# Kernel optimization log

Measured on AMD Instinct MI355X. Metric: run time of the kernel, lower is better.

Reference implementation:

```python
import jax, jax.numpy as jnp
import numpy as np

F8_MAX = 448.0  # float8_e4m3fn max
F4_MAX = 6.0    # fp4 e2m1 max
BLOCK = 16      # NVFP4 scaling block size along K

# representable |values| of fp4 e2m1 and midpoints for nearest rounding
_LEVELS = jnp.array([0.0, 0.5, 1.0, 1.5, 2.0, 3.0, 4.0, 6.0], dtype=jnp.float32)
_MIDS = (_LEVELS[:-1] + _LEVELS[1:]) * 0.5


def _e2m1_round(a):
    # round-to-nearest fp4 e2m1 value, sign-magnitude
    s = jnp.sign(a)
    m = jnp.clip(jnp.abs(a), 0.0, F4_MAX)
    idx = jnp.searchsorted(_MIDS, m, side='left')
    return s * jnp.take(_LEVELS, idx)


def _e4m3(x):
    # quantize to float8 e4m3 and dequantize back to fp32
    return jnp.clip(x, -F8_MAX, F8_MAX).astype(jnp.float8_e4m3fn).astype(jnp.float32)


def nvfp4_fake_quant(x, s2):
    # x: [..., K]; s2: scalar global scale = 448*6/global_amax
    shp = x.shape
    K = shp[-1]
    xb = x.reshape(shp[:-1] + (K // BLOCK, BLOCK))  # [..., K/16, 16]
    amax = jnp.max(jnp.abs(xb), axis=-1, keepdims=True)
    sf = _e4m3(amax * s2 / F4_MAX)          # stored per-block fp8 scale (cutlass_vec)
    scale = sf / s2                          # per-block dequant scale in real units
    safe = jnp.where(scale > 0.0, scale, 1.0)
    q = _e2m1_round(xb / safe)               # fp4 codes (as values)
    deq = jnp.where(scale > 0.0, q * scale, 0.0)
    return deq.reshape(shp)


def setup_inputs() -> dict:
    key = jax.random.key(0)
    kx, kw, kb, ks = jax.random.split(key, 4)
    K, N = 4096, 4096
    x = jax.random.normal(kx, (4, 2048, K), dtype=jnp.float32)
    weight = jax.random.uniform(kw, (N, K), dtype=jnp.float32)
    bias = jax.random.uniform(kb, (N,), dtype=jnp.float32)
    # fp4_global_scale of a rand(1, K) tensor, as done in the module __init__
    dummy = jax.random.uniform(ks, (1, K), dtype=jnp.float32)
    s_in2 = ((F8_MAX * F4_MAX) / jnp.max(jnp.abs(dummy))).reshape(1)
    return {'x': x, 'weight': weight, 'bias': bias, 's_in2': s_in2}


def reference(x, weight, bias, s_in2):
    s2_in = s_in2.reshape(())
    s2_w = (F8_MAX * F4_MAX) / jnp.max(jnp.abs(weight))  # fp4_global_scale(weight)
    x_dq = nvfp4_fake_quant(x, s2_in)        # fake-quant activations
    w_dq = nvfp4_fake_quant(weight, s2_w)    # dequantized fp4 weight (stored at init)
    # F.linear: [b,s,k] @ [n,k]^T + bias
    return jnp.einsum('bsk,nk->bsn', x_dq, w_dq) + bias
```

## Files before the change

kernel.cpp:

```cpp
#include <hip/hip_runtime.h>
#include <hip/hip_bf16.h>

typedef __attribute__((ext_vector_type(8))) short short8;
typedef __attribute__((ext_vector_type(8))) unsigned short ushort8;
typedef __attribute__((ext_vector_type(4))) float f32x4;
typedef unsigned short ushort;

#define K_DIM 4096
#define N_DIM 4096
#define BK 32
#define NT_TILES (K_DIM / BK)


__device__ __forceinline__ float e4m3_rne(float v) {
    if (v >= 0.015625f) {
        unsigned u = __float_as_uint(v);
        unsigned lsb = (u >> 20) & 1u;
        u = (u + 0x7FFFFu + lsb) & 0xFFF00000u;
        return __uint_as_float(u);
    }
    return rintf(v * 512.0f) * 0.001953125f;
}

__device__ __forceinline__ float e2m1_level(float m) {
    float lv = 0.0f;
    lv = (m > 0.25f) ? 0.5f : lv;
    lv = (m > 0.75f) ? 1.0f : lv;
    lv = (m > 1.25f) ? 1.5f : lv;
    lv = (m > 1.75f) ? 2.0f : lv;
    lv = (m > 2.5f)  ? 3.0f : lv;
    lv = (m > 3.5f)  ? 4.0f : lv;
    lv = (m > 5.0f)  ? 6.0f : lv;
    return lv;
}

__device__ __forceinline__ ushort f32_to_bf16_bits(float f) {
    unsigned u = __float_as_uint(f);
    return (ushort)((u + 0x7FFFu + ((u >> 16) & 1u)) >> 16);
}


__global__ void wamax_kernel(const float* __restrict__ w, unsigned* amax_bits, int n4) {
    float m = 0.f;
    const f32x4* w4 = (const f32x4*)w;
    for (int i = blockIdx.x * blockDim.x + threadIdx.x; i < n4; i += gridDim.x * blockDim.x) {
        f32x4 v = w4[i];
        m = fmaxf(m, fmaxf(fmaxf(fabsf(v.x), fabsf(v.y)), fmaxf(fabsf(v.z), fabsf(v.w))));
    }
#pragma unroll
    for (int off = 32; off >= 1; off >>= 1)
        m = fmaxf(m, __shfl_down(m, off));
    __shared__ float red[4];
    const int lane = threadIdx.x & 63, wv = threadIdx.x >> 6;
    if (lane == 0) red[wv] = m;
    __syncthreads();
    if (threadIdx.x == 0) {
        m = fmaxf(fmaxf(red[0], red[1]), fmaxf(red[2], red[3]));
        atomicMax(amax_bits, __float_as_uint(m));
    }
}

__global__ void quant16_kernel(const float* __restrict__ src,
                               const float* __restrict__ s2_ptr,
                               const unsigned* __restrict__ amax_bits,
                               ushort* __restrict__ dst, int nblk) {
    int t = blockIdx.x * blockDim.x + threadIdx.x;
    if (t >= nblk) return;
    float s2;
    if (s2_ptr) s2 = *s2_ptr;
    else        s2 = 2688.0f / __uint_as_float(*amax_bits);

    const f32x4* s = (const f32x4*)src + (size_t)t * 4;
    float vals[16];
    f32x4 v0 = s[0], v1 = s[1], v2 = s[2], v3 = s[3];
#pragma unroll
    for (int i = 0; i < 4; ++i) {
        vals[i] = v0[i]; vals[4 + i] = v1[i]; vals[8 + i] = v2[i]; vals[12 + i] = v3[i];
    }
    float amax = 0.f;
#pragma unroll
    for (int i = 0; i < 16; ++i) amax = fmaxf(amax, fabsf(vals[i]));

    float sf = e4m3_rne(fminf(amax * s2 / 6.0f, 448.0f));
    float scale = sf / s2;

    ushort8 o0, o1;
    if (scale > 0.f) {
#pragma unroll
        for (int i = 0; i < 16; ++i) {
            float r = vals[i] / scale;
            float m = fminf(fabsf(r), 6.0f);
            float q = copysignf(e2m1_level(m), r);
            ushort b = f32_to_bf16_bits(q * scale);
            if (i < 8) o0[i] = b; else o1[i - 8] = b;
        }
    } else {
#pragma unroll
        for (int i = 0; i < 8; ++i) { o0[i] = 0; o1[i] = 0; }
    }
    ushort8* d8 = (ushort8*)(dst + (size_t)t * 16);
    d8[0] = o0;
    d8[1] = o1;
}


__device__ __forceinline__ void gload16(const ushort* g, ushort* l) {
    __builtin_amdgcn_global_load_lds(
        (const __attribute__((address_space(1))) void*)g,
        (__attribute__((address_space(3))) void*)l, 16, 0, 0);
}

#define SYNC(N)                                              \
    asm volatile("s_waitcnt vmcnt(" #N ")" ::: "memory");    \
    __builtin_amdgcn_sched_barrier(0);                       \
    __builtin_amdgcn_s_barrier();                            \
    __builtin_amdgcn_sched_barrier(0)

__global__ __launch_bounds__(512, 2) void gemm8(
    const ushort* __restrict__ Aq, const ushort* __restrict__ Bq,
    const float* __restrict__ bias, float* __restrict__ C) {
    __shared__ ushort lds[4 * 16384];

    const int tid  = threadIdx.x;
    const int lane = tid & 63;
    const int wave = tid >> 6;
    const int wr = wave >> 2;
    const int wc = wave & 3;

    const int swz = blockIdx.x;
    const int g = swz >> 8, l = swz & 255;
    const int by = g * 16 + (l & 15);
    const int bx = l >> 4;
    const int bm = by * 256, bn = bx * 256;

    const int r0  = tid >> 2;
    const int cg0 = ((tid & 3) - ((r0 >> 1) & 3)) & 3;
    const ushort* sA0 = Aq + (size_t)(bm + r0) * K_DIM + cg0 * 8;
    const ushort* sB0 = Bq + (size_t)(bn + r0) * K_DIM + cg0 * 8;
    ushort* dA0 = &lds[wave * 512];
    ushort* dB0 = &lds[8192 + wave * 512];

    const int pr   = ((lane >> 4) + ((lane & 15) >> 1)) & 3;
    const int idxA = (wr * 128 + (lane & 15)) * 32 + pr * 8;
    const int idxB = 8192 + (wc * 64 + (lane & 15)) * 32 + pr * 8;

    f32x4 acc[8][4];
#pragma unroll
    for (int m = 0; m < 8; ++m)
#pragma unroll
        for (int n = 0; n < 4; ++n) acc[m][n] = (f32x4)(0.f);

#define STAGE(t) {                                                         \
        const size_t ko = (size_t)(t) * BK;                                \
        const int bb = ((t) & 3) * 16384;                                  \
        gload16(sA0 + ko,                          dA0 + bb);              \
        gload16(sA0 + (size_t)128 * K_DIM + ko,    dA0 + bb + 4096);       \
        gload16(sB0 + ko,                          dB0 + bb);              \
        gload16(sB0 + (size_t)128 * K_DIM + ko,    dB0 + bb + 4096); }

    auto compute = [&](int bufo) {
        const ushort* Lb = &lds[bufo];
        short8 af[8], bfr[4];
#pragma unroll
        for (int m = 0; m < 8; ++m) af[m]  = *(const short8*)(Lb + idxA + m * 512);
#pragma unroll
        for (int n = 0; n < 4; ++n) bfr[n] = *(const short8*)(Lb + idxB + n * 512);
#pragma unroll
        for (int m = 0; m < 8; ++m)
#pragma unroll
            for (int n = 0; n < 4; ++n)
                acc[m][n] = __builtin_amdgcn_mfma_f32_16x16x32_bf16(af[m], bfr[n], acc[m][n], 0, 0, 0);
    };

    STAGE(0); STAGE(1); STAGE(2);
    SYNC(8);

    for (int t = 0; t < NT_TILES - 3; ++t) {
        STAGE(t + 3);
        compute((t & 3) * 16384);
        SYNC(8);
    }
    compute(((NT_TILES - 3) & 3) * 16384);
    SYNC(4);
    compute(((NT_TILES - 2) & 3) * 16384);
    SYNC(0);
    compute(((NT_TILES - 1) & 3) * 16384);

    const int fq = lane >> 4, fr = lane & 15;
    float bv[4];
#pragma unroll
    for (int n = 0; n < 4; ++n) bv[n] = bias[bn + wc * 64 + n * 16 + fr];
#pragma unroll
    for (int m = 0; m < 8; ++m)
#pragma unroll
        for (int r = 0; r < 4; ++r) {
            const int row = bm + wr * 128 + m * 16 + fq * 4 + r;
            float* Cr = C + (size_t)row * N_DIM + bn + wc * 64 + fr;
#pragma unroll
            for (int n = 0; n < 4; ++n) Cr[n * 16] = acc[m][n][r] + bv[n];
        }
#undef STAGE
}


extern "C" void kernel_launch(void* const* d_in, const int* in_sizes, int n_in,
                              void* d_out, int out_size, void* d_ws, size_t ws_size,
                              hipStream_t stream) {
    const float* x     = (const float*)d_in[0];
    const float* w     = (const float*)d_in[1];
    const float* bias  = (const float*)d_in[2];
    const float* s_in2 = (const float*)d_in[3];
    float* out = (float*)d_out;

    const int M = in_sizes[0] / K_DIM;

    unsigned* amax_bits = (unsigned*)d_ws;
    ushort* xq = (ushort*)((char*)d_ws + 256);
    ushort* wq = (ushort*)((char*)d_ws + 256 + (size_t)M * K_DIM * 2);

    hipMemsetAsync(amax_bits, 0, 4, stream);
    wamax_kernel<<<1024, 256, 0, stream>>>(w, amax_bits, (N_DIM * K_DIM) / 4);

    const int nblk_x = (M * K_DIM) / 16;
    quant16_kernel<<<nblk_x / 256, 256, 0, stream>>>(x, s_in2, nullptr, xq, nblk_x);
    const int nblk_w = (N_DIM * K_DIM) / 16;
    quant16_kernel<<<nblk_w / 256, 256, 0, stream>>>(w, nullptr, amax_bits, wq, nblk_w);

    const int nwg = (M / 256) * (N_DIM / 256);
    gemm8<<<nwg, 512, 0, stream>>>(xq, wq, bias, out);
}
```

Measured before the change: 310.1 us.

## Restructure bf16 GEMM into double-buffered BK=64 pipeline with interleaved quarter-tile loads

The GEMM main loop moves from a 4-stage BK=32 ring buffer to a 2-stage BK=64 double buffer. Each K-tile's compute is split into four quadrant MFMA groups, and each group is interleaved with a quarter of the next tile's global-to-LDS loads plus fine-grained waitcnt and barriers. MFMA sections are raised in priority with s_setprio. The wave-to-output mapping changes to split 64-row by 32-col quadrants, with an 8-way XOR-like LDS swizzle for the wider tile. The aim is better overlap of memory and MFMA work and fewer barriers per unit of K, at the cost of more barriers per tile and less prefetch depth.

```diff
diff --git a/kernel.cpp b/kernel.cpp
--- a/kernel.cpp
+++ b/kernel.cpp
@@ -8,8 +8,8 @@
 
 #define K_DIM 4096
 #define N_DIM 4096
-#define BK 32
-#define NT_TILES (K_DIM / BK)
+#define BK 64
+#define NT (K_DIM / BK)
 
 
 __device__ __forceinline__ float e4m3_rne(float v) {
@@ -110,16 +110,15 @@
         (__attribute__((address_space(3))) void*)l, 16, 0, 0);
 }
 
-#define SYNC(N)                                              \
-    asm volatile("s_waitcnt vmcnt(" #N ")" ::: "memory");    \
-    __builtin_amdgcn_sched_barrier(0);                       \
-    __builtin_amdgcn_s_barrier();                            \
-    __builtin_amdgcn_sched_barrier(0)
+#define VM4 asm volatile("s_waitcnt vmcnt(4)" ::: "memory")
+#define VM2 asm volatile("s_waitcnt vmcnt(2)" ::: "memory")
+#define VM0 asm volatile("s_waitcnt vmcnt(0)" ::: "memory")
+#define BAR asm volatile("s_barrier" ::: "memory")
 
 __global__ __launch_bounds__(512, 2) void gemm8(
     const ushort* __restrict__ Aq, const ushort* __restrict__ Bq,
     const float* __restrict__ bias, float* __restrict__ C) {
-    __shared__ ushort lds[4 * 16384];
+    __shared__ ushort lds[2 * 32768];
 
     const int tid  = threadIdx.x;
     const int lane = tid & 63;
@@ -128,21 +127,24 @@
     const int wc = wave & 3;
 
     const int swz = blockIdx.x;
-    const int g = swz >> 8, l = swz & 255;
-    const int by = g * 16 + (l & 15);
-    const int bx = l >> 4;
+    const int grp = swz >> 8, lcl = swz & 255;
+    const int by = grp * 16 + (lcl & 15);
+    const int bx = lcl >> 4;
     const int bm = by * 256, bn = bx * 256;
 
-    const int r0  = tid >> 2;
-    const int cg0 = ((tid & 3) - ((r0 >> 1) & 3)) & 3;
-    const ushort* sA0 = Aq + (size_t)(bm + r0) * K_DIM + cg0 * 8;
-    const ushort* sB0 = Bq + (size_t)(bn + r0) * K_DIM + cg0 * 8;
-    ushort* dA0 = &lds[wave * 512];
-    ushort* dB0 = &lds[8192 + wave * 512];
-
-    const int pr   = ((lane >> 4) + ((lane & 15) >> 1)) & 3;
-    const int idxA = (wr * 128 + (lane & 15)) * 32 + pr * 8;
-    const int idxB = 8192 + (wc * 64 + (lane & 15)) * 32 + pr * 8;
+    const int r0  = tid >> 3;
+    const int cg0 = ((tid & 7) - ((r0 >> 1) & 7)) & 7;
+    const ushort* sA = Aq + (size_t)(bm + r0) * K_DIM + cg0 * 8;
+    const ushort* sB = Bq + (size_t)(bn + r0) * K_DIM + cg0 * 8;
+    ushort* dst0 = &lds[tid * 8];
+
+    const int rowA = wr * 64 + (lane & 15);
+    const int rowB = wc * 32 + (lane & 15);
+    const int ksl  = lane >> 4;
+    const int baseA[2] = { rowA * 64 + ((((ksl) + (rowA >> 1)) & 7) << 3),
+                           rowA * 64 + (((4 + ksl + (rowA >> 1)) & 7) << 3) };
+    const int baseB[2] = { 16384 + rowB * 64 + ((((ksl) + (rowB >> 1)) & 7) << 3),
+                           16384 + rowB * 64 + (((4 + ksl + (rowB >> 1)) & 7) << 3) };
 
     f32x4 acc[8][4];
 #pragma unroll
@@ -150,56 +152,102 @@
 #pragma unroll
         for (int n = 0; n < 4; ++n) acc[m][n] = (f32x4)(0.f);
 
-#define STAGE(t) {                                                         \
-        const size_t ko = (size_t)(t) * BK;                                \
-        const int bb = ((t) & 3) * 16384;                                  \
-        gload16(sA0 + ko,                          dA0 + bb);              \
-        gload16(sA0 + (size_t)128 * K_DIM + ko,    dA0 + bb + 4096);       \
-        gload16(sB0 + ko,                          dB0 + bb);              \
-        gload16(sB0 + (size_t)128 * K_DIM + ko,    dB0 + bb + 4096); }
-
-    auto compute = [&](int bufo) {
-        const ushort* Lb = &lds[bufo];
-        short8 af[8], bfr[4];
-#pragma unroll
-        for (int m = 0; m < 8; ++m) af[m]  = *(const short8*)(Lb + idxA + m * 512);
-#pragma unroll
-        for (int n = 0; n < 4; ++n) bfr[n] = *(const short8*)(Lb + idxB + n * 512);
-#pragma unroll
-        for (int m = 0; m < 8; ++m)
+    short8 af[4][2], bfr[4][2];
+
+#define SA0(t) { const size_t ko = (size_t)(t) * BK; ushort* d = dst0 + ((t) & 1) * 32768;         \
+    gload16(sA + ko, d); gload16(sA + (size_t)64 * K_DIM + ko, d + 4096); }
+#define SA1(t) { const size_t ko = (size_t)(t) * BK; ushort* d = dst0 + ((t) & 1) * 32768 + 8192;  \
+    gload16(sA + (size_t)128 * K_DIM + ko, d); gload16(sA + (size_t)192 * K_DIM + ko, d + 4096); }
+#define SB0(t) { const size_t ko = (size_t)(t) * BK; ushort* d = dst0 + ((t) & 1) * 32768 + 16384; \
+    gload16(sB + ko, d); gload16(sB + (size_t)64 * K_DIM + ko, d + 4096); }
+#define SB1(t) { const size_t ko = (size_t)(t) * BK; ushort* d = dst0 + ((t) & 1) * 32768 + 24576; \
+    gload16(sB + (size_t)128 * K_DIM + ko, d); gload16(sB + (size_t)192 * K_DIM + ko, d + 4096); }
+
+#define READ_A(mh, Lb)                                                        \
+    _Pragma("unroll") for (int m = 0; m < 4; ++m) {                           \
+        af[m][0] = *(const short8*)((Lb) + (mh) * 8192 + m * 1024 + baseA[0]); \
+        af[m][1] = *(const short8*)((Lb) + (mh) * 8192 + m * 1024 + baseA[1]); }
+#define READ_B(nh, Lb)                                                        \
+    _Pragma("unroll") for (int n = 0; n < 2; ++n) {                           \
+        bfr[(nh)*2 + n][0] = *(const short8*)((Lb) + (nh) * 8192 + n * 1024 + baseB[0]); \
+        bfr[(nh)*2 + n][1] = *(const short8*)((Lb) + (nh) * 8192 + n * 1024 + baseB[1]); }
+
+#define MM(m0, n0)                                                            \
+    __builtin_amdgcn_s_setprio(1);                                            \
+    _Pragma("unroll") for (int m = 0; m < 4; ++m)                             \
+    _Pragma("unroll") for (int n = 0; n < 2; ++n)                             \
+    _Pragma("unroll") for (int ks = 0; ks < 2; ++ks)                          \
+        acc[(m0) + m][(n0) + n] = __builtin_amdgcn_mfma_f32_16x16x32_bf16(    \
+            af[m][ks], bfr[(n0) + n][ks], acc[(m0) + m][(n0) + n], 0, 0, 0);  \
+    __builtin_amdgcn_s_setprio(0);
+
+    SA0(0); SB0(0); SB1(0); SA1(0);
+    VM4; BAR;
+
+#pragma unroll 1
+    for (int t = 0; t < NT - 1; ++t) {
+        const ushort* Lb = &lds[(t & 1) * 32768];
+        READ_A(0, Lb); READ_B(0, Lb);
+        SA0(t + 1);
+        VM4; BAR;
+        MM(0, 0);
+        BAR;
+        READ_B(1, Lb);
+        SB0(t + 1);
+        VM4; BAR;
+        MM(0, 2);
+        BAR;
+        READ_A(1, Lb);
+        SB1(t + 1);
+        BAR;
+        MM(4, 0);
+        BAR;
+        SA1(t + 1);
+        VM4; BAR;
+        MM(4, 2);
+        BAR;
+    }
+    {
+        const ushort* Lb = &lds[((NT - 1) & 1) * 32768];
+        READ_A(0, Lb); READ_B(0, Lb);
+        VM2; BAR;
+        MM(0, 0);
+        BAR;
+        READ_B(1, Lb);
+        VM0; BAR;
+        MM(0, 2);
+        BAR;
+        READ_A(1, Lb);
+        BAR;
+        MM(4, 0);
+        BAR;
+        BAR;
+        MM(4, 2);
+        BAR;
+    }
+
+    const int fq = lane >> 4, fr = lane & 15;
+    const int colb = bn + wc * 32 + fr;
+    float bv[4];
+#pragma unroll
+    for (int n = 0; n < 4; ++n) bv[n] = bias[colb + (n >> 1) * 128 + (n & 1) * 16];
+#pragma unroll
+    for (int m = 0; m < 8; ++m)
+#pragma unroll
+        for (int r = 0; r < 4; ++r) {
+            const int row = bm + (m >> 2) * 128 + wr * 64 + (m & 3) * 16 + fq * 4 + r;
+            float* Cr = C + (size_t)row * N_DIM + colb;
 #pragma unroll
             for (int n = 0; n < 4; ++n)
-                acc[m][n] = __builtin_amdgcn_mfma_f32_16x16x32_bf16(af[m], bfr[n], acc[m][n], 0, 0, 0);
-    };
-
-    STAGE(0); STAGE(1); STAGE(2);
-    SYNC(8);
-
-    for (int t = 0; t < NT_TILES - 3; ++t) {
-        STAGE(t + 3);
-        compute((t & 3) * 16384);
-        SYNC(8);
-    }
-    compute(((NT_TILES - 3) & 3) * 16384);
-    SYNC(4);
-    compute(((NT_TILES - 2) & 3) * 16384);
-    SYNC(0);
-    compute(((NT_TILES - 1) & 3) * 16384);
-
-    const int fq = lane >> 4, fr = lane & 15;
-    float bv[4];
-#pragma unroll
-    for (int n = 0; n < 4; ++n) bv[n] = bias[bn + wc * 64 + n * 16 + fr];
-#pragma unroll
-    for (int m = 0; m < 8; ++m)
-#pragma unroll
-        for (int r = 0; r < 4; ++r) {
-            const int row = bm + wr * 128 + m * 16 + fq * 4 + r;
-            float* Cr = C + (size_t)row * N_DIM + bn + wc * 64 + fr;
-#pragma unroll
-            for (int n = 0; n < 4; ++n) Cr[n * 16] = acc[m][n][r] + bv[n];
+                Cr[(n >> 1) * 128 + (n & 1) * 16] = acc[m][n][r] + bv[n];
         }
-#undef STAGE
+#undef SA0
+#undef SA1
+#undef SB0
+#undef SB1
+#undef READ_A
+#undef READ_B
+#undef MM
 }
 
 
```

New measurement: 322.3 us. 4.0% more time.

## Software-pipeline LDS fragment reads with MFMA halves and split global loads

Applied to the files above, without the earlier changes.

Restructures the GEMM main loop so the LDS fragment reads for the next half-tile and tile are issued while the current MFMA half runs. The code uses finer lgkmcnt and vmcnt waits, a single barrier per tile, and interleaves the A and B global-to-LDS loads between the two MFMA halves. It also raises wave priority around the MFMA blocks with s_setprio. The intent is to hide LDS read latency and reduce barrier stalls. The cost is more fragile wait-count reasoning and a possible race on buffer reuse.

```diff
diff --git a/kernel.cpp b/kernel.cpp
--- a/kernel.cpp
+++ b/kernel.cpp
@@ -9,7 +9,7 @@
 #define K_DIM 4096
 #define N_DIM 4096
 #define BK 32
-#define NT_TILES (K_DIM / BK)
+#define NT (K_DIM / BK)
 
 
 __device__ __forceinline__ float e4m3_rne(float v) {
@@ -110,11 +110,13 @@
         (__attribute__((address_space(3))) void*)l, 16, 0, 0);
 }
 
-#define SYNC(N)                                              \
-    asm volatile("s_waitcnt vmcnt(" #N ")" ::: "memory");    \
-    __builtin_amdgcn_sched_barrier(0);                       \
-    __builtin_amdgcn_s_barrier();                            \
-    __builtin_amdgcn_sched_barrier(0)
+#define VM4 asm volatile("s_waitcnt vmcnt(4)" ::: "memory")
+#define VM0 asm volatile("s_waitcnt vmcnt(0)" ::: "memory")
+#define LG4 do { asm volatile("s_waitcnt lgkmcnt(4)" ::: "memory"); \
+                 __builtin_amdgcn_sched_barrier(0); } while (0)
+#define LG0 do { asm volatile("s_waitcnt lgkmcnt(0)" ::: "memory"); \
+                 __builtin_amdgcn_sched_barrier(0); } while (0)
+#define BAR asm volatile("s_barrier" ::: "memory")
 
 __global__ __launch_bounds__(512, 2) void gemm8(
     const ushort* __restrict__ Aq, const ushort* __restrict__ Bq,
@@ -128,9 +130,9 @@
     const int wc = wave & 3;
 
     const int swz = blockIdx.x;
-    const int g = swz >> 8, l = swz & 255;
-    const int by = g * 16 + (l & 15);
-    const int bx = l >> 4;
+    const int grp = swz >> 8, lcl = swz & 255;
+    const int by = grp * 16 + (lcl & 15);
+    const int bx = lcl >> 4;
     const int bm = by * 256, bn = bx * 256;
 
     const int r0  = tid >> 2;
@@ -150,41 +152,78 @@
 #pragma unroll
         for (int n = 0; n < 4; ++n) acc[m][n] = (f32x4)(0.f);
 
-#define STAGE(t) {                                                         \
-        const size_t ko = (size_t)(t) * BK;                                \
-        const int bb = ((t) & 3) * 16384;                                  \
-        gload16(sA0 + ko,                          dA0 + bb);              \
-        gload16(sA0 + (size_t)128 * K_DIM + ko,    dA0 + bb + 4096);       \
-        gload16(sB0 + ko,                          dB0 + bb);              \
-        gload16(sB0 + (size_t)128 * K_DIM + ko,    dB0 + bb + 4096); }
-
-    auto compute = [&](int bufo) {
-        const ushort* Lb = &lds[bufo];
-        short8 af[8], bfr[4];
-#pragma unroll
-        for (int m = 0; m < 8; ++m) af[m]  = *(const short8*)(Lb + idxA + m * 512);
-#pragma unroll
-        for (int n = 0; n < 4; ++n) bfr[n] = *(const short8*)(Lb + idxB + n * 512);
-#pragma unroll
-        for (int m = 0; m < 8; ++m)
-#pragma unroll
-            for (int n = 0; n < 4; ++n)
-                acc[m][n] = __builtin_amdgcn_mfma_f32_16x16x32_bf16(af[m], bfr[n], acc[m][n], 0, 0, 0);
-    };
-
-    STAGE(0); STAGE(1); STAGE(2);
-    SYNC(8);
-
-    for (int t = 0; t < NT_TILES - 3; ++t) {
-        STAGE(t + 3);
-        compute((t & 3) * 16384);
-        SYNC(8);
-    }
-    compute(((NT_TILES - 3) & 3) * 16384);
-    SYNC(4);
-    compute(((NT_TILES - 2) & 3) * 16384);
-    SYNC(0);
-    compute(((NT_TILES - 1) & 3) * 16384);
+    short8 af[8], bfr[4];
+
+#define SA(t) { const size_t ko = (size_t)(t) * BK; const int bb = ((t) & 3) * 16384; \
+    gload16(sA0 + ko, dA0 + bb); gload16(sA0 + (size_t)128 * K_DIM + ko, dA0 + bb + 4096); }
+#define SB(t) { const size_t ko = (size_t)(t) * BK; const int bb = ((t) & 3) * 16384; \
+    gload16(sB0 + ko, dB0 + bb); gload16(sB0 + (size_t)128 * K_DIM + ko, dB0 + bb + 4096); }
+
+#define READ_ALO(bb) _Pragma("unroll") for (int m = 0; m < 4; ++m) \
+        af[m] = *(const short8*)&lds[(bb) + idxA + m * 512];
+#define READ_AHI(bb) _Pragma("unroll") for (int m = 0; m < 4; ++m) \
+        af[4 + m] = *(const short8*)&lds[(bb) + idxA + (4 + m) * 512];
+#define READ_B(bb)   _Pragma("unroll") for (int n = 0; n < 4; ++n) \
+        bfr[n] = *(const short8*)&lds[(bb) + idxB + n * 512];
+
+#define MML                                                                   \
+    __builtin_amdgcn_s_setprio(1);                                            \
+    _Pragma("unroll") for (int m = 0; m < 4; ++m)                             \
+    _Pragma("unroll") for (int n = 0; n < 4; ++n)                             \
+        acc[m][n] = __builtin_amdgcn_mfma_f32_16x16x32_bf16(af[m], bfr[n], acc[m][n], 0, 0, 0); \
+    __builtin_amdgcn_s_setprio(0);
+#define MMH                                                                   \
+    __builtin_amdgcn_s_setprio(1);                                            \
+    _Pragma("unroll") for (int m = 4; m < 8; ++m)                             \
+    _Pragma("unroll") for (int n = 0; n < 4; ++n)                             \
+        acc[m][n] = __builtin_amdgcn_mfma_f32_16x16x32_bf16(af[m], bfr[n], acc[m][n], 0, 0, 0); \
+    __builtin_amdgcn_s_setprio(0);
+
+    SA(0); SB(0); SA(1); SB(1); SA(2); SB(2);
+    VM4; BAR;
+    READ_ALO(0); READ_B(0);
+
+#pragma unroll 1
+    for (int t = 0; t <= NT - 4; ++t) {
+        const int bb  = (t & 3) * 16384;
+        const int bb1 = ((t + 1) & 3) * 16384;
+        VM4; BAR;
+        READ_AHI(bb);
+        SA(t + 3);
+        LG4;
+        MML;
+        READ_ALO(bb1);
+        SB(t + 3);
+        LG4;
+        MMH;
+        READ_B(bb1);
+    }
+    {
+        const int bb  = ((NT - 3) & 3) * 16384;
+        const int bb1 = ((NT - 2) & 3) * 16384;
+        VM4; BAR;
+        READ_AHI(bb);
+        LG4; MML;
+        READ_ALO(bb1);
+        LG4; MMH;
+        READ_B(bb1);
+    }
+    {
+        const int bb  = ((NT - 2) & 3) * 16384;
+        const int bb1 = ((NT - 1) & 3) * 16384;
+        VM0; BAR;
+        READ_AHI(bb);
+        LG4; MML;
+        READ_ALO(bb1);
+        LG4; MMH;
+        READ_B(bb1);
+    }
+    {
+        const int bb = ((NT - 1) & 3) * 16384;
+        READ_AHI(bb);
+        LG4; MML;
+        LG0; MMH;
+    }
 
     const int fq = lane >> 4, fr = lane & 15;
     float bv[4];
@@ -199,7 +238,13 @@
 #pragma unroll
             for (int n = 0; n < 4; ++n) Cr[n * 16] = acc[m][n][r] + bv[n];
         }
-#undef STAGE
+#undef SA
+#undef SB
+#undef READ_ALO
+#undef READ_AHI
+#undef READ_B
+#undef MML
+#undef MMH
 }
 
 
```

Result: faster. 297.7 us (-4.0%).

## Shrink GEMM tile to 128x256 with 3-stage LDS pipeline and interleaved MFMA waits

Applied to the files above, without the earlier changes.

Halves the M tile to 128 rows, giving each wave a 4x4 MFMA accumulator, and drops from a 4-buffer to a 3-buffer LDS ring so occupancy can rise to 4 workgroups per CU. The main loop is restructured so LDS fragment reads are issued before the next global-to-LDS stage, and MFMAs are split into groups gated by lgkmcnt waits with setprio raised around them. This targets better latency hiding and occupancy, at the cost of lower arithmetic intensity per tile, since B tiles are reloaded twice as often.

```diff
diff --git a/kernel.cpp b/kernel.cpp
--- a/kernel.cpp
+++ b/kernel.cpp
@@ -9,7 +9,7 @@
 #define K_DIM 4096
 #define N_DIM 4096
 #define BK 32
-#define NT_TILES (K_DIM / BK)
+#define NT (K_DIM / BK)
 
 
 __device__ __forceinline__ float e4m3_rne(float v) {
@@ -110,16 +110,19 @@
         (__attribute__((address_space(3))) void*)l, 16, 0, 0);
 }
 
-#define SYNC(N)                                              \
-    asm volatile("s_waitcnt vmcnt(" #N ")" ::: "memory");    \
-    __builtin_amdgcn_sched_barrier(0);                       \
-    __builtin_amdgcn_s_barrier();                            \
-    __builtin_amdgcn_sched_barrier(0)
-
-__global__ __launch_bounds__(512, 2) void gemm8(
+#define VM3 asm volatile("s_waitcnt vmcnt(3)" ::: "memory")
+#define VM0 asm volatile("s_waitcnt vmcnt(0)" ::: "memory")
+#define LGW(N) do { asm volatile("s_waitcnt lgkmcnt(" #N ")" ::: "memory"); \
+                    __builtin_amdgcn_sched_barrier(0); } while (0)
+#define BAR asm volatile("s_barrier" ::: "memory")
+
+#define BUFSZ 12288
+#define BOFF_B 4096
+
+__global__ __launch_bounds__(512, 4) void gemm8(
     const ushort* __restrict__ Aq, const ushort* __restrict__ Bq,
     const float* __restrict__ bias, float* __restrict__ C) {
-    __shared__ ushort lds[4 * 16384];
+    __shared__ ushort lds[3 * BUFSZ];
 
     const int tid  = threadIdx.x;
     const int lane = tid & 63;
@@ -128,78 +131,97 @@
     const int wc = wave & 3;
 
     const int swz = blockIdx.x;
-    const int g = swz >> 8, l = swz & 255;
-    const int by = g * 16 + (l & 15);
-    const int bx = l >> 4;
-    const int bm = by * 256, bn = bx * 256;
+    const int grp = swz >> 8, lcl = swz & 255;
+    const int by = grp * 16 + (lcl & 15);
+    const int bx = lcl >> 4;
+    const int bm = by * 128, bn = bx * 256;
 
     const int r0  = tid >> 2;
     const int cg0 = ((tid & 3) - ((r0 >> 1) & 3)) & 3;
     const ushort* sA0 = Aq + (size_t)(bm + r0) * K_DIM + cg0 * 8;
     const ushort* sB0 = Bq + (size_t)(bn + r0) * K_DIM + cg0 * 8;
-    ushort* dA0 = &lds[wave * 512];
-    ushort* dB0 = &lds[8192 + wave * 512];
+    ushort* dA0 = &lds[tid * 8];
+    ushort* dB0 = &lds[BOFF_B + tid * 8];
 
     const int pr   = ((lane >> 4) + ((lane & 15) >> 1)) & 3;
-    const int idxA = (wr * 128 + (lane & 15)) * 32 + pr * 8;
-    const int idxB = 8192 + (wc * 64 + (lane & 15)) * 32 + pr * 8;
-
-    f32x4 acc[8][4];
-#pragma unroll
-    for (int m = 0; m < 8; ++m)
+    const int idxA = (wr * 64 + (lane & 15)) * 32 + pr * 8;
+    const int idxB = BOFF_B + (wc * 64 + (lane & 15)) * 32 + pr * 8;
+
+    f32x4 acc[4][4];
+#pragma unroll
+    for (int m = 0; m < 4; ++m)
 #pragma unroll
         for (int n = 0; n < 4; ++n) acc[m][n] = (f32x4)(0.f);
 
-#define STAGE(t) {                                                         \
-        const size_t ko = (size_t)(t) * BK;                                \
-        const int bb = ((t) & 3) * 16384;                                  \
-        gload16(sA0 + ko,                          dA0 + bb);              \
-        gload16(sA0 + (size_t)128 * K_DIM + ko,    dA0 + bb + 4096);       \
-        gload16(sB0 + ko,                          dB0 + bb);              \
-        gload16(sB0 + (size_t)128 * K_DIM + ko,    dB0 + bb + 4096); }
-
-    auto compute = [&](int bufo) {
-        const ushort* Lb = &lds[bufo];
-        short8 af[8], bfr[4];
-#pragma unroll
-        for (int m = 0; m < 8; ++m) af[m]  = *(const short8*)(Lb + idxA + m * 512);
-#pragma unroll
-        for (int n = 0; n < 4; ++n) bfr[n] = *(const short8*)(Lb + idxB + n * 512);
-#pragma unroll
-        for (int m = 0; m < 8; ++m)
-#pragma unroll
-            for (int n = 0; n < 4; ++n)
-                acc[m][n] = __builtin_amdgcn_mfma_f32_16x16x32_bf16(af[m], bfr[n], acc[m][n], 0, 0, 0);
-    };
-
-    STAGE(0); STAGE(1); STAGE(2);
-    SYNC(8);
-
-    for (int t = 0; t < NT_TILES - 3; ++t) {
-        STAGE(t + 3);
-        compute((t & 3) * 16384);
-        SYNC(8);
-    }
-    compute(((NT_TILES - 3) & 3) * 16384);
-    SYNC(4);
-    compute(((NT_TILES - 2) & 3) * 16384);
-    SYNC(0);
-    compute(((NT_TILES - 1) & 3) * 16384);
+    short8 af[4], bfr[4];
+
+#define STAGE(t, bb) {                                                        \
+        const size_t ko = (size_t)(t) * BK;                                   \
+        gload16(sA0 + ko, dA0 + (bb));                                        \
+        gload16(sB0 + ko, dB0 + (bb));                                        \
+        gload16(sB0 + (size_t)128 * K_DIM + ko, dB0 + (bb) + 4096); }
+
+#define TILE(bb, STAGE_STMT, VMW)                                             \
+    {                                                                         \
+        VMW; BAR;                                                             \
+        _Pragma("unroll") for (int m = 0; m < 4; ++m)                         \
+            af[m] = *(const short8*)&lds[(bb) + idxA + m * 512];              \
+        _Pragma("unroll") for (int n = 0; n < 4; ++n)                         \
+            bfr[n] = *(const short8*)&lds[(bb) + idxB + n * 512];             \
+        STAGE_STMT;                                                           \
+        LGW(3);                                                               \
+        __builtin_amdgcn_s_setprio(1);                                        \
+        _Pragma("unroll") for (int m = 0; m < 4; ++m)                         \
+            acc[m][0] = __builtin_amdgcn_mfma_f32_16x16x32_bf16(af[m], bfr[0], acc[m][0], 0, 0, 0); \
+        __builtin_amdgcn_s_setprio(0);                                        \
+        LGW(2);                                                               \
+        __builtin_amdgcn_s_setprio(1);                                        \
+        _Pragma("unroll") for (int m = 0; m < 4; ++m)                         \
+            acc[m][1] = __builtin_amdgcn_mfma_f32_16x16x32_bf16(af[m], bfr[1], acc[m][1], 0, 0, 0); \
+        __builtin_amdgcn_s_setprio(0);                                        \
+        LGW(1);                                                               \
+        __builtin_amdgcn_s_setprio(1);                                        \
+        _Pragma("unroll") for (int m = 0; m < 4; ++m)                         \
+            acc[m][2] = __builtin_amdgcn_mfma_f32_16x16x32_bf16(af[m], bfr[2], acc[m][2], 0, 0, 0); \
+        __builtin_amdgcn_s_setprio(0);                                        \
+        LGW(0);                                                               \
+        __builtin_amdgcn_s_setprio(1);                                        \
+        _Pragma("unroll") for (int m = 0; m < 4; ++m)                         \
+            acc[m][3] = __builtin_amdgcn_mfma_f32_16x16x32_bf16(af[m], bfr[3], acc[m][3], 0, 0, 0); \
+        __builtin_amdgcn_s_setprio(0);                                        \
+    }
+
+#define NOPS ((void)0)
+
+    STAGE(0, 0); STAGE(1, BUFSZ);
+
+#pragma unroll 1
+    for (int u = 0; u < (NT - 2) / 3; ++u) {
+        const int t0 = u * 3;
+        TILE(0,         STAGE(t0 + 2, 2 * BUFSZ), VM3);
+        TILE(BUFSZ,     STAGE(t0 + 3, 0),         VM3);
+        TILE(2 * BUFSZ, STAGE(t0 + 4, BUFSZ),     VM3);
+    }
+    TILE(0,     NOPS, VM3);
+    TILE(BUFSZ, NOPS, VM0);
 
     const int fq = lane >> 4, fr = lane & 15;
+    const int colb = bn + wc * 64 + fr;
     float bv[4];
 #pragma unroll
-    for (int n = 0; n < 4; ++n) bv[n] = bias[bn + wc * 64 + n * 16 + fr];
-#pragma unroll
-    for (int m = 0; m < 8; ++m)
+    for (int n = 0; n < 4; ++n) bv[n] = bias[colb + n * 16];
+#pragma unroll
+    for (int m = 0; m < 4; ++m)
 #pragma unroll
         for (int r = 0; r < 4; ++r) {
-            const int row = bm + wr * 128 + m * 16 + fq * 4 + r;
-            float* Cr = C + (size_t)row * N_DIM + bn + wc * 64 + fr;
+            const int row = bm + wr * 64 + m * 16 + fq * 4 + r;
+            float* Cr = C + (size_t)row * N_DIM + colb;
 #pragma unroll
             for (int n = 0; n < 4; ++n) Cr[n * 16] = acc[m][n][r] + bv[n];
         }
 #undef STAGE
+#undef TILE
+#undef NOPS
 }
 
 
@@ -226,6 +248,6 @@
     const int nblk_w = (N_DIM * K_DIM) / 16;
     quant16_kernel<<<nblk_w / 256, 256, 0, stream>>>(w, nullptr, amax_bits, wq, nblk_w);
 
-    const int nwg = (M / 256) * (N_DIM / 256);
+    const int nwg = (M / 128) * (N_DIM / 256);
     gemm8<<<nwg, 512, 0, stream>>>(xq, wq, bias, out);
 }
```

New measurement: 336.1 us. 1.08x slower.
